# Optimization experiments

Hardware: AMD Instinct MI355X
Metric: run time of the kernel (lower is better)

Reference implementation:

```python
import jax, jax.numpy as jnp
import numpy as np

IN_DIM = 512
OUT_DIM = 512


def setup_inputs() -> dict:
    key = jax.random.key(0)
    ks = jax.random.split(key, 7)
    B, S = 4, 2048
    scale = 1.0 / np.sqrt(IN_DIM)
    X = jax.random.normal(ks[0], (B, S, IN_DIM), dtype=jnp.float32)
    Wq = jax.random.normal(ks[1], (IN_DIM, OUT_DIM), dtype=jnp.float32) * scale
    Wk = jax.random.normal(ks[2], (IN_DIM, OUT_DIM), dtype=jnp.float32) * scale
    Wv = jax.random.normal(ks[3], (IN_DIM, OUT_DIM), dtype=jnp.float32) * scale
    bq = jnp.zeros((OUT_DIM,), dtype=jnp.float32)
    bk = jnp.zeros((OUT_DIM,), dtype=jnp.float32)
    bv = jnp.zeros((OUT_DIM,), dtype=jnp.float32)
    return {"X": X, "Wq": Wq, "bq": bq, "Wk": Wk, "bk": bk, "Wv": Wv, "bv": bv}


def reference(X, Wq, bq, Wk, bk, Wv, bv):
    # Q/K/V projections: [B,S,in] @ [in,out] -> [B,S,out]
    Q = X @ Wq + bq
    K = X @ Wk + bk
    V = X @ Wv + bv
    d_k = jnp.asarray(Q.shape[-1], Q.dtype)
    # scores: [B,S,S] = QK^T / sqrt(d_k)
    scores = jnp.einsum('bsd,btd->bst', Q, K) / jnp.sqrt(d_k)
    attn = jax.nn.softmax(scores, axis=-1)
    # out: [B,S,out]
    return jnp.einsum('bst,btd->bsd', attn, V)
```

## Files before the change

kernel.cpp:

```cpp
#include <hip/hip_runtime.h>
#include <hip/hip_bf16.h>
#include <stdint.h>

#define SEQ   2048
#define DIM   512
#define BATCH 4

typedef __attribute__((ext_vector_type(8))) short  short8;
typedef __attribute__((ext_vector_type(4))) float  floatx4;

static __device__ __forceinline__ unsigned short f2b(float f) {
  return __builtin_bit_cast(unsigned short, __float2bfloat16(f));
}

static __device__ __forceinline__ void gll16(const void* g, void* l) {
  __builtin_amdgcn_global_load_lds(
      (__attribute__((address_space(1))) void*)(uintptr_t)g,
      (__attribute__((address_space(3))) void*)l, 16, 0, 0);
}


template <int AF, int BF, int WM, int WN, int KC, int PH, int KIT>
__device__ __forceinline__ void fgemm_8p(
    const char* __restrict__ A, int rtA0, int TKA,
    const char* __restrict__ B, int rtB0, int TKB,
    char* lds, floatx4 (&acc)[AF / WM][BF / WN])
{
  constexpr int AWF  = AF / WM, BWF = BF / WN;
  constexpr int SLOT = (AF + BF) * KC * 1024;
  constexpr int L    = KC * (AF / 8 + BF / 8);
  constexpr int AC   = AWF / PH;
  static_assert(KIT >= 3, "pipeline needs >=3 K-slots");
  static_assert(AWF % PH == 0 && L % PH == 0, "phase split must divide");
  const int tid = threadIdx.x;
  const int w = tid >> 6, l = tid & 63;
  const int wm = w % WM, wn = w / WM;

  auto stage_part = [&](int slot, int kt, int p) {
    char* dst = lds + slot * SLOT;
#pragma unroll
    for (int g = p * (L / PH); g < (p + 1) * (L / PH); ++g) {
      if (g < KC * (AF / 8)) {
        const int c = g / (AF / 8), q = g % (AF / 8);
        const int f = q * 8 + w;
        gll16(A + (((size_t)(rtA0 + f) * TKA + kt * KC + c) << 10) + l * 16,
              dst + (c * AF + f) * 1024 + l * 16);
      } else {
        const int h = g - KC * (AF / 8);
        const int c = h / (BF / 8), q = h % (BF / 8);
        const int f = q * 8 + w;
        gll16(B + (((size_t)(rtB0 + f) * TKB + kt * KC + c) << 10) + l * 16,
              dst + (KC * AF + c * BF + f) * 1024 + l * 16);
      }
    }
  };
  auto stage_all = [&](int slot, int kt) {
#pragma unroll
    for (int p = 0; p < PH; ++p) stage_part(slot, kt, p);
  };

  stage_all(0, 0); stage_all(1, 1); stage_all(2, 2);
  asm volatile("s_waitcnt vmcnt(%0) lgkmcnt(0)\ns_barrier" :: "n"(2 * L) : "memory");

  short8 bf[KC][BWF];
#pragma unroll 4
  for (int kt = 0; kt < KIT; ++kt) {
    const char* bA = lds + (kt & 3) * SLOT;
    const char* bB = bA + KC * AF * 1024;
#pragma unroll
    for (int p = 0; p < PH; ++p) {
      short8 af[KC][AC];
#pragma unroll
      for (int c = 0; c < KC; ++c)
#pragma unroll
        for (int i = 0; i < AC; ++i)
          af[c][i] = *(const short8*)(bA + (c * AF + wm * AWF + p * AC + i) * 1024 + l * 16);
      if (p == 0) {
#pragma unroll
        for (int c = 0; c < KC; ++c)
#pragma unroll
          for (int j = 0; j < BWF; ++j)
            bf[c][j] = *(const short8*)(bB + (c * BF + wn * BWF + j) * 1024 + l * 16);
      }
      if (kt + 3 < KIT) stage_part((kt + 3) & 3, kt + 3, p);

      asm volatile("s_barrier" ::: "memory");
      asm volatile("s_waitcnt lgkmcnt(0)" ::: "memory");
      __builtin_amdgcn_s_setprio(1);
#pragma unroll
      for (int c = 0; c < KC; ++c)
#pragma unroll
        for (int i = 0; i < AC; ++i)
#pragma unroll
          for (int j = 0; j < BWF; ++j)
            acc[p * AC + i][j] = __builtin_amdgcn_mfma_f32_16x16x32_bf16(
                af[c][i], bf[c][j], acc[p * AC + i][j], 0, 0, 0);
      __builtin_amdgcn_s_setprio(0);

      if (p == PH - 1) {
        if (kt + 3 < KIT)
          asm volatile("s_waitcnt vmcnt(%0)\ns_barrier" :: "n"(2 * L) : "memory");
        else if (kt + 2 < KIT)
          asm volatile("s_waitcnt vmcnt(%0)\ns_barrier" :: "n"(L) : "memory");
        else if (kt + 1 < KIT)
          asm volatile("s_waitcnt vmcnt(0)\ns_barrier" ::: "memory");
      } else {
        asm volatile("s_barrier" ::: "memory");
      }
    }
  }
}

__global__ __launch_bounds__(256) void setup_kernel(
    const float* __restrict__ X, const float* __restrict__ Wq,
    const float* __restrict__ Wk, const float* __restrict__ Wv,
    short8* __restrict__ XbF, short8* __restrict__ WF)
{
  const int flat = blockIdx.x * 256 + threadIdx.x;
  {
    const int tile = flat >> 6, l = flat & 63;
    const int row = (tile >> 4) * 16 + (l & 15);
    const int k0  = (tile & 15) * 32 + (l >> 4) * 8;
    const float4 v0 = *(const float4*)(X + (size_t)row * DIM + k0);
    const float4 v1 = *(const float4*)(X + (size_t)row * DIM + k0 + 4);
    short8 o;
    o[0] = (short)f2b(v0.x); o[1] = (short)f2b(v0.y);
    o[2] = (short)f2b(v0.z); o[3] = (short)f2b(v0.w);
    o[4] = (short)f2b(v1.x); o[5] = (short)f2b(v1.y);
    o[6] = (short)f2b(v1.z); o[7] = (short)f2b(v1.w);
    XbF[flat] = o;
  }
  if (flat < 3 * 32768) {
    const int z = flat >> 15, within = flat & 32767;
    const float* W = (z == 0) ? Wq : (z == 1) ? Wk : Wv;
    const int tile = within >> 6, l = within & 63;
    const int n  = (tile >> 4) * 16 + (l & 15);
    const int k0 = (tile & 15) * 32 + (l >> 4) * 8;
    short8 o;
#pragma unroll
    for (int e = 0; e < 8; ++e)
      o[e] = (short)f2b(W[(size_t)(k0 + e) * DIM + n]);
    WF[flat] = o;
  }
}

__global__ __launch_bounds__(512, 2) void qkv_kernel(
    const short8* __restrict__ XbF, const short8* __restrict__ WF,
    const float* __restrict__ bq, const float* __restrict__ bk,
    const float* __restrict__ bv,
    unsigned short* __restrict__ QF, unsigned short* __restrict__ KF,
    unsigned short* __restrict__ VF)
{
  __shared__ char lds[131072];
  const int n = blockIdx.x;
  const int xcd = n & 7, i = n >> 3;
  const int x = xcd + 8 * (i & 3);
  const int zy = i >> 2;
  const int z = zy >> 1, y = zy & 1;
  const int lane = threadIdx.x & 63, w = threadIdx.x >> 6;
  const int wm = w & 1, wn = w >> 1;
  const char* Xc = (const char*)XbF;
  const char* Wc = (const char*)WF;
  floatx4 acc[8][4] = {};

  if (z < 2) {
    fgemm_8p<16, 16, 2, 4, 1, 2, 16>(Wc + (size_t)z * 524288, y * 16, 16,
                                     Xc, x * 16, 16, lds, acc);
    const float* bias = z ? bk : bq;
    unsigned short* OF = z ? KF : QF;
    const int dbase = y * 256 + wm * 128;
    const int sbase = x * 256 + wn * 64;
#pragma unroll
    for (int i2 = 0; i2 < 8; ++i2) {
      const int d0 = dbase + i2 * 16 + (lane >> 4) * 4;
      const float4 b4 = *(const float4*)(bias + d0);
#pragma unroll
      for (int j = 0; j < 4; ++j) {
        const int s = sbase + j * 16 + (lane & 15);
        ushort4 pk;
        pk.x = f2b(acc[i2][j][0] + b4.x);
        pk.y = f2b(acc[i2][j][1] + b4.y);
        pk.z = f2b(acc[i2][j][2] + b4.z);
        pk.w = f2b(acc[i2][j][3] + b4.w);
        *(ushort4*)(OF + (size_t)((s >> 4) * 16 + (d0 >> 5)) * 512 +
                    ((((d0 & 31) >> 3) << 4) | (s & 15)) * 8 + (d0 & 7)) = pk;
      }
    }
  } else {
    fgemm_8p<16, 16, 2, 4, 1, 2, 16>(Xc, x * 16, 16,
                                     Wc + 2 * 524288, y * 16, 16, lds, acc);
    const int sbase = x * 256 + wm * 128;
    const int dbase = y * 256 + wn * 64;
#pragma unroll
    for (int i2 = 0; i2 < 8; ++i2) {
      const int s0 = sbase + i2 * 16 + (lane >> 4) * 4;
      const int bt = s0 >> 11, t0 = s0 & 2047;
#pragma unroll
      for (int j = 0; j < 4; ++j) {
        const int d = dbase + j * 16 + (lane & 15);
        const float bn = bv[d];
        ushort4 pk;
        pk.x = f2b(acc[i2][j][0] + bn);
        pk.y = f2b(acc[i2][j][1] + bn);
        pk.z = f2b(acc[i2][j][2] + bn);
        pk.w = f2b(acc[i2][j][3] + bn);
        *(ushort4*)(VF + (size_t)bt * DIM * SEQ +
                    (size_t)((d >> 4) * 64 + (t0 >> 5)) * 512 +
                    ((((t0 & 31) >> 3) << 4) | (d & 15)) * 8 + (t0 & 7)) = pk;
      }
    }
  }
}

__global__ __launch_bounds__(512, 2) void scores_kernel(
    const unsigned short* __restrict__ QF, const unsigned short* __restrict__ KF,
    unsigned short* __restrict__ ScF, float* __restrict__ prow)
{
  __shared__ char lds[131072];
  const int n = blockIdx.x;
  const int xcd = n & 7, i = n >> 3;
  const int b = xcd >> 1;
  const int x = (xcd & 1) * 4 + (i & 3);
  const int y = i >> 2;
  const int lane = threadIdx.x & 63, w = threadIdx.x >> 6;
  const int wm = w & 1, wn = w >> 1;
  floatx4 acc[8][4] = {};
  fgemm_8p<16, 16, 2, 4, 1, 2, 16>((const char*)KF + (size_t)b * 2097152, y * 16, 16,
                                   (const char*)QF + (size_t)b * 2097152, x * 16, 16,
                                   lds, acc);

  unsigned short* S = ScF + (size_t)b * SEQ * SEQ;
  const float scale = 0.044194173824159216f;
  const int tbase = y * 256 + wm * 128;
  const int sbase = x * 256 + wn * 64;
  float colsum[4] = {0.f, 0.f, 0.f, 0.f};
#pragma unroll
  for (int i2 = 0; i2 < 8; ++i2) {
    const int t0 = tbase + i2 * 16 + (lane >> 4) * 4;
#pragma unroll
    for (int j = 0; j < 4; ++j) {
      const int s = sbase + j * 16 + (lane & 15);
      float e0 = __expf(acc[i2][j][0] * scale);
      float e1 = __expf(acc[i2][j][1] * scale);
      float e2 = __expf(acc[i2][j][2] * scale);
      float e3 = __expf(acc[i2][j][3] * scale);
      colsum[j] += (e0 + e1) + (e2 + e3);
      ushort4 pk;
      pk.x = f2b(e0); pk.y = f2b(e1); pk.z = f2b(e2); pk.w = f2b(e3);
      *(ushort4*)(S + (size_t)((s >> 4) * 64 + (t0 >> 5)) * 512 +
                  ((((t0 & 31) >> 3) << 4) | (s & 15)) * 8 + (t0 & 7)) = pk;
    }
  }
#pragma unroll
  for (int j = 0; j < 4; ++j) {
    colsum[j] += __shfl_xor(colsum[j], 16, 64);
    colsum[j] += __shfl_xor(colsum[j], 32, 64);
  }
  if (lane < 16) {
    float* dst = prow + ((size_t)(y * 2 + wm) * BATCH + b) * SEQ + sbase + lane;
#pragma unroll
    for (int j = 0; j < 4; ++j) dst[j * 16] = colsum[j];
  }
}

__global__ __launch_bounds__(512, 2) void pv_kernel(
    const unsigned short* __restrict__ ScF, const unsigned short* __restrict__ VF,
    const float* __restrict__ prow, float* __restrict__ out)
{
  __shared__ char lds[131072];
  __shared__ float rinv[128];
  const int n = blockIdx.x;
  const int xcd = n & 7, i = n >> 3;
  const int b = xcd >> 1;
  const int x = (xcd & 1) * 8 + (i & 7);
  const int y = i >> 3;
  const int t = threadIdx.x;
  if (t < 128) {
    const int s = x * 128 + t;
    float r = 0.f;
#pragma unroll
    for (int q = 0; q < 16; ++q) r += prow[((size_t)q * BATCH + b) * SEQ + s];
    rinv[t] = 1.f / r;
  }
  const int lane = threadIdx.x & 63, w = threadIdx.x >> 6;
  const int wm = w & 1, wn = w >> 1;
  floatx4 acc[4][2] = {};
  fgemm_8p<8, 8, 2, 4, 2, 1, 32>((const char*)ScF + (size_t)b * 8388608, x * 8, 64,
                                 (const char*)VF + (size_t)b * 2097152, y * 8, 64,
                                 lds, acc);

  const int mbase = x * 128 + wm * 64;
  const int dbase = y * 128 + wn * 32;
#pragma unroll
  for (int i2 = 0; i2 < 4; ++i2) {
    const int r0 = wm * 64 + i2 * 16 + (lane >> 4) * 4;
    const int m0 = mbase + i2 * 16 + (lane >> 4) * 4;
    const float inv0 = rinv[r0], inv1 = rinv[r0 + 1], inv2 = rinv[r0 + 2], inv3 = rinv[r0 + 3];
#pragma unroll
    for (int j = 0; j < 2; ++j) {
      const int d = dbase + j * 16 + (lane & 15);
      float* o = out + ((size_t)b * SEQ + m0) * DIM + d;
      o[0 * DIM] = acc[i2][j][0] * inv0;
      o[1 * DIM] = acc[i2][j][1] * inv1;
      o[2 * DIM] = acc[i2][j][2] * inv2;
      o[3 * DIM] = acc[i2][j][3] * inv3;
    }
  }
}

extern "C" void kernel_launch(void* const* d_in, const int* in_sizes, int n_in,
                              void* d_out, int out_size, void* d_ws, size_t ws_size,
                              hipStream_t stream) {
  const float* X  = (const float*)d_in[0];
  const float* Wq = (const float*)d_in[1];
  const float* bq = (const float*)d_in[2];
  const float* Wk = (const float*)d_in[3];
  const float* bk = (const float*)d_in[4];
  const float* Wv = (const float*)d_in[5];
  const float* bv = (const float*)d_in[6];
  float* out = (float*)d_out;
  char* ws = (char*)d_ws;

  short8* XbF = (short8*)(ws + 0);
  float*  prow = (float*)(ws + 0);
  short8* WF  = (short8*)(ws + 8388608);
  unsigned short* QF  = (unsigned short*)(ws + 9961472);
  unsigned short* KF  = (unsigned short*)(ws + 18350080);
  unsigned short* VF  = (unsigned short*)(ws + 26738688);
  unsigned short* ScF = (unsigned short*)(ws + 35127296);

  setup_kernel<<<dim3(2048), 256, 0, stream>>>(X, Wq, Wk, Wv, XbF, WF);
  qkv_kernel<<<dim3(192), 512, 0, stream>>>(XbF, WF, bq, bk, bv, QF, KF, VF);
  scores_kernel<<<dim3(256), 512, 0, stream>>>(QF, KF, ScF, prow);
  pv_kernel<<<dim3(256), 512, 0, stream>>>(ScF, VF, prow, out);
}
```

Measured before the change: 142.8 us.

## Halve GEMM block tiles to 4 waves with 3-slot pipeline, doubling grid size

Generalises the fragment GEMM to a configurable wave count and moves from a 4-slot to a 3-slot LDS ring with two K-slices prefetched instead of three. The qkv, scores and pv kernels now use 256-thread blocks with half-width N tiles and about 72KB of LDS. Grids double (384/512/512 blocks) and block-to-XCD mapping is reworked, so each of the 256 CUs gets more than one block. In exchange, per-block operand reuse drops and prefetch depth is shallower, which raises global/L2 traffic and exposes more load latency.

```diff
diff --git a/kernel.cpp b/kernel.cpp
--- a/kernel.cpp
+++ b/kernel.cpp
@@ -20,53 +20,55 @@
 }
 
 
-template <int AF, int BF, int WM, int WN, int KC, int PH, int KIT>
-__device__ __forceinline__ void fgemm_8p(
+template <int AF, int BF, int WM, int WN, int KC, int PH, int KIT, int NW>
+__device__ __forceinline__ void fgemm_p(
     const char* __restrict__ A, int rtA0, int TKA,
     const char* __restrict__ B, int rtB0, int TKB,
     char* lds, floatx4 (&acc)[AF / WM][BF / WN])
 {
   constexpr int AWF  = AF / WM, BWF = BF / WN;
   constexpr int SLOT = (AF + BF) * KC * 1024;
-  constexpr int L    = KC * (AF / 8 + BF / 8);
+  constexpr int L    = KC * (AF / NW + BF / NW);
   constexpr int AC   = AWF / PH;
   static_assert(KIT >= 3, "pipeline needs >=3 K-slots");
+  static_assert(AF % NW == 0 && BF % NW == 0, "frag rows must divide waves");
   static_assert(AWF % PH == 0 && L % PH == 0, "phase split must divide");
   const int tid = threadIdx.x;
   const int w = tid >> 6, l = tid & 63;
   const int wm = w % WM, wn = w / WM;
 
-  auto stage_part = [&](int slot, int kt, int p) {
-    char* dst = lds + slot * SLOT;
+  auto stage_part = [&](char* dst, int kt, int p) {
 #pragma unroll
     for (int g = p * (L / PH); g < (p + 1) * (L / PH); ++g) {
-      if (g < KC * (AF / 8)) {
-        const int c = g / (AF / 8), q = g % (AF / 8);
-        const int f = q * 8 + w;
+      if (g < KC * (AF / NW)) {
+        const int c = g / (AF / NW), q = g % (AF / NW);
+        const int f = q * NW + w;
         gll16(A + (((size_t)(rtA0 + f) * TKA + kt * KC + c) << 10) + l * 16,
               dst + (c * AF + f) * 1024 + l * 16);
       } else {
-        const int h = g - KC * (AF / 8);
-        const int c = h / (BF / 8), q = h % (BF / 8);
-        const int f = q * 8 + w;
+        const int h = g - KC * (AF / NW);
+        const int c = h / (BF / NW), q = h % (BF / NW);
+        const int f = q * NW + w;
         gll16(B + (((size_t)(rtB0 + f) * TKB + kt * KC + c) << 10) + l * 16,
               dst + (KC * AF + c * BF + f) * 1024 + l * 16);
       }
     }
   };
-  auto stage_all = [&](int slot, int kt) {
-#pragma unroll
-    for (int p = 0; p < PH; ++p) stage_part(slot, kt, p);
-  };
-
-  stage_all(0, 0); stage_all(1, 1); stage_all(2, 2);
-  asm volatile("s_waitcnt vmcnt(%0) lgkmcnt(0)\ns_barrier" :: "n"(2 * L) : "memory");
+
+#pragma unroll
+  for (int p = 0; p < PH; ++p) stage_part(lds, 0, p);
+#pragma unroll
+  for (int p = 0; p < PH; ++p) stage_part(lds + SLOT, 1, p);
+  asm volatile("s_waitcnt vmcnt(%0) lgkmcnt(0)\ns_barrier" :: "n"(L) : "memory");
 
   short8 bf[KC][BWF];
-#pragma unroll 4
+  int cs = 0;
+#pragma unroll 2
   for (int kt = 0; kt < KIT; ++kt) {
-    const char* bA = lds + (kt & 3) * SLOT;
+    const char* bA = lds + cs * SLOT;
     const char* bB = bA + KC * AF * 1024;
+    int ns = cs - 1; if (ns < 0) ns = 2;
+    char* pdst = lds + ns * SLOT;
 #pragma unroll
     for (int p = 0; p < PH; ++p) {
       short8 af[KC][AC];
@@ -82,7 +84,7 @@
           for (int j = 0; j < BWF; ++j)
             bf[c][j] = *(const short8*)(bB + (c * BF + wn * BWF + j) * 1024 + l * 16);
       }
-      if (kt + 3 < KIT) stage_part((kt + 3) & 3, kt + 3, p);
+      if (kt + 2 < KIT) stage_part(pdst, kt + 2, p);
 
       asm volatile("s_barrier" ::: "memory");
       asm volatile("s_waitcnt lgkmcnt(0)" ::: "memory");
@@ -98,9 +100,7 @@
       __builtin_amdgcn_s_setprio(0);
 
       if (p == PH - 1) {
-        if (kt + 3 < KIT)
-          asm volatile("s_waitcnt vmcnt(%0)\ns_barrier" :: "n"(2 * L) : "memory");
-        else if (kt + 2 < KIT)
+        if (kt + 2 < KIT)
           asm volatile("s_waitcnt vmcnt(%0)\ns_barrier" :: "n"(L) : "memory");
         else if (kt + 1 < KIT)
           asm volatile("s_waitcnt vmcnt(0)\ns_barrier" ::: "memory");
@@ -108,6 +108,7 @@
         asm volatile("s_barrier" ::: "memory");
       }
     }
+    ++cs; if (cs == 3) cs = 0;
   }
 }
 
@@ -144,32 +145,30 @@
   }
 }
 
-__global__ __launch_bounds__(512, 2) void qkv_kernel(
+__global__ __launch_bounds__(256, 2) void qkv_kernel(
     const short8* __restrict__ XbF, const short8* __restrict__ WF,
     const float* __restrict__ bq, const float* __restrict__ bk,
     const float* __restrict__ bv,
     unsigned short* __restrict__ QF, unsigned short* __restrict__ KF,
     unsigned short* __restrict__ VF)
 {
-  __shared__ char lds[131072];
-  const int n = blockIdx.x;
-  const int xcd = n & 7, i = n >> 3;
-  const int x = xcd + 8 * (i & 3);
-  const int zy = i >> 2;
-  const int z = zy >> 1, y = zy & 1;
+  __shared__ char lds[73728];
+  const int blk = blockIdx.x;
+  const int n = (blk & 7) * 48 + (blk >> 3);
   const int lane = threadIdx.x & 63, w = threadIdx.x >> 6;
   const int wm = w & 1, wn = w >> 1;
   const char* Xc = (const char*)XbF;
   const char* Wc = (const char*)WF;
   floatx4 acc[8][4] = {};
 
-  if (z < 2) {
-    fgemm_8p<16, 16, 2, 4, 1, 2, 16>(Wc + (size_t)z * 524288, y * 16, 16,
-                                     Xc, x * 16, 16, lds, acc);
+  if (n < 256) {
+    const int z = n >> 7, y = (n >> 6) & 1, x = n & 63;
+    fgemm_p<16, 8, 2, 2, 1, 2, 16, 4>(Wc + (size_t)z * 524288, y * 16, 16,
+                                      Xc, x * 8, 16, lds, acc);
     const float* bias = z ? bk : bq;
     unsigned short* OF = z ? KF : QF;
     const int dbase = y * 256 + wm * 128;
-    const int sbase = x * 256 + wn * 64;
+    const int sbase = x * 128 + wn * 64;
 #pragma unroll
     for (int i2 = 0; i2 < 8; ++i2) {
       const int d0 = dbase + i2 * 16 + (lane >> 4) * 4;
@@ -187,10 +186,12 @@
       }
     }
   } else {
-    fgemm_8p<16, 16, 2, 4, 1, 2, 16>(Xc, x * 16, 16,
-                                     Wc + 2 * 524288, y * 16, 16, lds, acc);
+    const int m = n - 256;
+    const int x = m >> 2, y = m & 3;
+    fgemm_p<16, 8, 2, 2, 1, 2, 16, 4>(Xc, x * 16, 16,
+                                      Wc + 2 * 524288, y * 8, 16, lds, acc);
     const int sbase = x * 256 + wm * 128;
-    const int dbase = y * 256 + wn * 64;
+    const int dbase = y * 128 + wn * 64;
 #pragma unroll
     for (int i2 = 0; i2 < 8; ++i2) {
       const int s0 = sbase + i2 * 16 + (lane >> 4) * 4;
@@ -212,27 +213,26 @@
   }
 }
 
-__global__ __launch_bounds__(512, 2) void scores_kernel(
+__global__ __launch_bounds__(256, 2) void scores_kernel(
     const unsigned short* __restrict__ QF, const unsigned short* __restrict__ KF,
     unsigned short* __restrict__ ScF, float* __restrict__ prow)
 {
-  __shared__ char lds[131072];
-  const int n = blockIdx.x;
-  const int xcd = n & 7, i = n >> 3;
-  const int b = xcd >> 1;
-  const int x = (xcd & 1) * 4 + (i & 3);
-  const int y = i >> 2;
+  __shared__ char lds[73728];
+  const int blk = blockIdx.x;
+  const int n = (blk & 7) * 64 + (blk >> 3);
+  const int b = n >> 7, t = n & 127;
+  const int y = t >> 4, x = t & 15;
   const int lane = threadIdx.x & 63, w = threadIdx.x >> 6;
   const int wm = w & 1, wn = w >> 1;
   floatx4 acc[8][4] = {};
-  fgemm_8p<16, 16, 2, 4, 1, 2, 16>((const char*)KF + (size_t)b * 2097152, y * 16, 16,
-                                   (const char*)QF + (size_t)b * 2097152, x * 16, 16,
-                                   lds, acc);
+  fgemm_p<16, 8, 2, 2, 1, 2, 16, 4>((const char*)KF + (size_t)b * 2097152, y * 16, 16,
+                                    (const char*)QF + (size_t)b * 2097152, x * 8, 16,
+                                    lds, acc);
 
   unsigned short* S = ScF + (size_t)b * SEQ * SEQ;
   const float scale = 0.044194173824159216f;
   const int tbase = y * 256 + wm * 128;
-  const int sbase = x * 256 + wn * 64;
+  const int sbase = x * 128 + wn * 64;
   float colsum[4] = {0.f, 0.f, 0.f, 0.f};
 #pragma unroll
   for (int i2 = 0; i2 < 8; ++i2) {
@@ -263,34 +263,33 @@
   }
 }
 
-__global__ __launch_bounds__(512, 2) void pv_kernel(
+__global__ __launch_bounds__(256, 2) void pv_kernel(
     const unsigned short* __restrict__ ScF, const unsigned short* __restrict__ VF,
     const float* __restrict__ prow, float* __restrict__ out)
 {
-  __shared__ char lds[131072];
+  __shared__ char lds[73728];
   __shared__ float rinv[128];
-  const int n = blockIdx.x;
-  const int xcd = n & 7, i = n >> 3;
-  const int b = xcd >> 1;
-  const int x = (xcd & 1) * 8 + (i & 7);
-  const int y = i >> 3;
+  const int blk = blockIdx.x;
+  const int n = (blk & 7) * 64 + (blk >> 3);
+  const int b = n >> 7, r = n & 127;
+  const int x = r >> 3, y = r & 7;
   const int t = threadIdx.x;
   if (t < 128) {
     const int s = x * 128 + t;
-    float r = 0.f;
-#pragma unroll
-    for (int q = 0; q < 16; ++q) r += prow[((size_t)q * BATCH + b) * SEQ + s];
-    rinv[t] = 1.f / r;
+    float rr = 0.f;
+#pragma unroll
+    for (int q = 0; q < 16; ++q) rr += prow[((size_t)q * BATCH + b) * SEQ + s];
+    rinv[t] = 1.f / rr;
   }
   const int lane = threadIdx.x & 63, w = threadIdx.x >> 6;
   const int wm = w & 1, wn = w >> 1;
   floatx4 acc[4][2] = {};
-  fgemm_8p<8, 8, 2, 4, 2, 1, 32>((const char*)ScF + (size_t)b * 8388608, x * 8, 64,
-                                 (const char*)VF + (size_t)b * 2097152, y * 8, 64,
-                                 lds, acc);
+  fgemm_p<8, 4, 2, 2, 2, 1, 32, 4>((const char*)ScF + (size_t)b * 8388608, x * 8, 64,
+                                   (const char*)VF + (size_t)b * 2097152, y * 4, 64,
+                                   lds, acc);
 
   const int mbase = x * 128 + wm * 64;
-  const int dbase = y * 128 + wn * 32;
+  const int dbase = y * 64 + wn * 32;
 #pragma unroll
   for (int i2 = 0; i2 < 4; ++i2) {
     const int r0 = wm * 64 + i2 * 16 + (lane >> 4) * 4;
@@ -330,7 +329,7 @@
   unsigned short* ScF = (unsigned short*)(ws + 35127296);
 
   setup_kernel<<<dim3(2048), 256, 0, stream>>>(X, Wq, Wk, Wv, XbF, WF);
-  qkv_kernel<<<dim3(192), 512, 0, stream>>>(XbF, WF, bq, bk, bv, QF, KF, VF);
-  scores_kernel<<<dim3(256), 512, 0, stream>>>(QF, KF, ScF, prow);
-  pv_kernel<<<dim3(256), 512, 0, stream>>>(ScF, VF, prow, out);
-}
+  qkv_kernel<<<dim3(384), 256, 0, stream>>>(XbF, WF, bq, bk, bv, QF, KF, VF);
+  scores_kernel<<<dim3(512), 256, 0, stream>>>(QF, KF, ScF, prow);
+  pv_kernel<<<dim3(512), 256, 0, stream>>>(ScF, VF, prow, out);
+}
```

Result: faster. 137.7 us (-3.5%).
